# Kernel tuning notes

Measured on AMD Instinct MI355X. Metric: run time of the kernel, lower is better.

## Reference

```python
import jax, jax.numpy as jnp
import numpy as np

B, CIN, W = 4, 3, 28          # batch, in_channels, image size (= max_pos_embedding)
MID, HEADS, G, COUT = 16, 8, 4, 64
HALF = MID // 2               # row / col embedding dims


def _embed(u, w1, b1, gamma, beta, w2, b2):
    """Positional-embedding MLP applied elementwise to scalars u (N,).
    Conv2d(1->16,k=1) -> LayerNorm(16 channels) -> Swish -> Conv2d(16->MID/2,k=1)."""
    h = u[:, None] * w1[None, :] + b1                     # (N, 16)
    mu = h.mean(-1, keepdims=True)
    var = ((h - mu) ** 2).mean(-1, keepdims=True)
    h = gamma * (h - mu) / jnp.sqrt(var + 1e-5) + beta    # LayerNorm over channels
    h = h * jax.nn.sigmoid(h)                             # Swish
    return h @ w2.T + b2                                  # (N, HALF)


def _rot_indices():
    """Acted relative-position lookup indices for the 4 rotations.
    Values index into u = concat(rel, -rel) where rel = linspace(-1,1,2W-1)."""
    n = 2 * W - 1
    ar = np.arange(W)
    rel = ar[None, :] - ar[:, None] + (W - 1)             # rel[i,k] in [0, 2W-2]
    R = np.broadcast_to(rel[:, None, :, None], (W,) * 4)  # depends on (i,k)
    C = np.broadcast_to(rel[None, :, None, :], (W,) * 4)  # depends on (j,l)
    # rotation by 0/90/180/270 deg acting on (row, col) relative coordinates
    ridx = np.stack([R, C + n, R + n, C], 0)              # row component index
    cidx = np.stack([C, R, C + n, R + n], 0)              # col component index
    return jnp.asarray(ridx, jnp.int32), jnp.asarray(cidx, jnp.int32)


def setup_inputs() -> dict:
    key = jax.random.key(0)
    ks = jax.random.split(key, 24)
    def nrm(k, shape, fan):
        return jax.random.normal(k, shape, jnp.float32) / np.float32(np.sqrt(fan))
    inp = {"x": jax.random.normal(ks[0], (B, CIN, W, W), jnp.float32)}
    inp["wq"] = nrm(ks[1], (MID * HEADS, CIN), CIN); inp["bq"] = jnp.zeros((MID * HEADS,), jnp.float32)
    inp["wk"] = nrm(ks[2], (MID * HEADS, CIN), CIN); inp["bk"] = jnp.zeros((MID * HEADS,), jnp.float32)
    inp["wv"] = nrm(ks[3], (MID * HEADS, CIN), CIN); inp["bv"] = jnp.zeros((MID * HEADS,), jnp.float32)
    inp["w_out"] = nrm(ks[4], (COUT, MID * HEADS), MID * HEADS); inp["b_out"] = jnp.zeros((COUT,), jnp.float32)
    for pfx, base in (("row", 5), ("col", 12)):
        inp[f"{pfx}_w1"] = nrm(ks[base], (16,), 1)
        inp[f"{pfx}_b1"] = jnp.zeros((16,), jnp.float32)
        inp[f"{pfx}_gamma"] = jnp.ones((16,), jnp.float32)
        inp[f"{pfx}_beta"] = jnp.zeros((16,), jnp.float32)
        inp[f"{pfx}_w2"] = nrm(ks[base + 1], (HALF, 16), 16)
        inp[f"{pfx}_b2"] = jnp.zeros((HALF,), jnp.float32)
    inp["ridx"], inp["cidx"] = _rot_indices()
    return inp


def reference(x, wq, bq, wk, bk, wv, bv, w_out, b_out,
              row_w1, row_b1, row_gamma, row_beta, row_w2, row_b2,
              col_w1, col_b1, col_gamma, col_beta, col_w2, col_b2,
              ridx, cidx):
    b, c, H, Wd = x.shape
    # 1x1-conv q/k/v, viewed as (b, mid, heads, H, W)
    q = (jnp.einsum('oc,bcij->boij', wq, x) + bq[:, None, None]).reshape(b, MID, HEADS, H, Wd)
    k_ = (jnp.einsum('oc,bcij->boij', wk, x) + bk[:, None, None]).reshape(b, MID, HEADS, H, Wd)
    v = (jnp.einsum('oc,bcij->boij', wv, x) + bv[:, None, None]).reshape(b, MID, HEADS, H, Wd)

    content = jnp.einsum('bmhij,bmhkl->bhijkl', q, k_)     # (b,h,i,j,k,l)

    lin = jnp.linspace(-1.0, 1.0, 2 * Wd - 1)
    u = jnp.concatenate([lin, -lin])                       # unique relative coords
    E_row = _embed(u, row_w1, row_b1, row_gamma, row_beta, row_w2, row_b2)
    E_col = _embed(u, col_w1, col_b1, col_gamma, col_beta, col_w2, col_b2)
    row_emb = E_row[ridx]                                  # (G,i,j,k,l,HALF)
    col_emb = E_col[cidx]

    scores = jnp.einsum('bmhij,gijklm->bhgijkl', q[:, :HALF], row_emb)
    scores = scores + jnp.einsum('bmhij,gijklm->bhgijkl', q[:, HALF:], col_emb)
    scores = (scores + content[:, :, None]) / np.float32(np.sqrt(c))

    sh = scores.shape                                      # softmax over flattened (k,l)
    probs = jax.nn.softmax(scores.reshape(sh[:-2] + (-1,)), axis=-1).reshape(sh)

    out_v = jnp.einsum('bhgijkl,bmhkl->bmhgij', probs, v)  # (b,mid,heads,G,i,j)
    out_v = out_v.reshape(b, MID * HEADS, G, H, Wd)
    out = jnp.einsum('om,bmgij->bogij', w_out, out_v) + b_out[:, None, None, None]
    return out
```

## Files before the change

kernel.cpp:

```cpp
#include <hip/hip_runtime.h>
#include <hip/hip_fp16.h>

#define NPOS 784
#define WDIM 28

typedef _Float16 f16x8 __attribute__((ext_vector_type(8)));
typedef _Float16 f16x4 __attribute__((ext_vector_type(4)));
typedef float    f32x4 __attribute__((ext_vector_type(4)));

__global__ __launch_bounds__(256) void prep_kernel(
    const float* __restrict__ x,
    const float* __restrict__ wq, const float* __restrict__ bq,
    const float* __restrict__ wk, const float* __restrict__ bk,
    const float* __restrict__ wv, const float* __restrict__ bv,
    const float* __restrict__ w_out,
    const float* __restrict__ rw1, const float* __restrict__ rb1,
    const float* __restrict__ rga, const float* __restrict__ rbe,
    const float* __restrict__ rw2, const float* __restrict__ rb2,
    const float* __restrict__ cw1, const float* __restrict__ cb1,
    const float* __restrict__ cga, const float* __restrict__ cbe,
    const float* __restrict__ cw2, const float* __restrict__ cb2,
    float* __restrict__ Qf32, _Float16* __restrict__ Qfrag,
    _Float16* __restrict__ Kfrag, _Float16* __restrict__ Vfrag,
    _Float16* __restrict__ Wfrag,
    float* __restrict__ Etr, float* __restrict__ Etc)
{
    const int t = threadIdx.x;
    if (blockIdx.x == 416) {
        int d = -1;
        const float *w1 = rw1, *b1 = rb1, *ga = rga, *be = rbe, *w2 = rw2, *b2 = rb2;
        float* E = Etr;
        if (t < 110) { d = t; }
        else if (t >= 128 && t < 238) { d = t - 128; w1 = cw1; b1 = cb1; ga = cga; be = cbe; w2 = cw2; b2 = cb2; E = Etc; }
        if (d < 0) return;
        float u = (d < 55) ? (-1.0f + (float)d * (2.0f / 54.0f))
                           : -(-1.0f + (float)(d - 55) * (2.0f / 54.0f));
        float hb[16], mu = 0.0f;
#pragma unroll
        for (int c = 0; c < 16; ++c) { hb[c] = u * w1[c] + b1[c]; mu += hb[c]; }
        mu *= (1.0f / 16.0f);
        float var = 0.0f;
#pragma unroll
        for (int c = 0; c < 16; ++c) { float dv = hb[c] - mu; var += dv * dv; }
        var *= (1.0f / 16.0f);
        float rstd = rsqrtf(var + 1e-5f);
#pragma unroll
        for (int c = 0; c < 16; ++c) {
            float hn = ga[c] * (hb[c] - mu) * rstd + be[c];
            hb[c] = hn / (1.0f + __expf(-hn));
        }
#pragma unroll
        for (int m = 0; m < 8; ++m) {
            float e = b2[m];
#pragma unroll
            for (int c = 0; c < 16; ++c) e += hb[c] * w2[m * 16 + c];
            E[m * 110 + d] = e;
        }
        return;
    }
    if (blockIdx.x == 417) {
        for (int idx = t; idx < 8192; idx += 256) {
            int obc = idx >> 9, lane = (idx >> 3) & 63, j = idx & 7;
            int o  = (obc >> 2) * 16 + (lane & 15);
            int mh = (obc & 3) * 32 + (lane >> 4) * 8 + j;
            Wfrag[idx] = (_Float16)w_out[o * 128 + mh];
        }
        return;
    }

    const int bid  = blockIdx.x;
    const int b    = bid / 104, rem = bid - b * 104;
    const int tile = rem >> 3, h = rem & 7;
    const int lane = t & 63, mg = t >> 6;
    const int bh   = b * 8 + h;

    {
        int which = t >> 7, sub = (t >> 5) & 3, l32 = 32 + (t & 31);
        int qz = tile * 4 + sub;
        if (qz < 49) {
            _Float16* dst = (which ? Kfrag : Qfrag) + ((size_t)(bh * 49 + qz) * 64 + l32) * 8;
            *(f16x8*)dst = (f16x8){};
        }
        if (tile == 12 && t < 32)
            *(f16x8*)(Vfrag + ((size_t)(bh * 25 + 24) * 64 + 32 + t) * 8) = (f16x8){};
    }

    const int ij = tile * 64 + lane;
    if (ij >= NPOS) return;

    float x0 = x[(b * 3 + 0) * NPOS + ij];
    float x1 = x[(b * 3 + 1) * NPOS + ij];
    float x2 = x[(b * 3 + 2) * NPOS + ij];

    float4 qv, kv;
    float vv[4];
#pragma unroll
    for (int j = 0; j < 4; ++j) {
        int m = mg * 4 + j, oc = m * 8 + h;
        float w0, w1, w2v;
        w0 = wq[oc*3+0]; w1 = wq[oc*3+1]; w2v = wq[oc*3+2];
        ((float*)&qv)[j] = bq[oc] + w0*x0 + w1*x1 + w2v*x2;
        w0 = wk[oc*3+0]; w1 = wk[oc*3+1]; w2v = wk[oc*3+2];
        ((float*)&kv)[j] = bk[oc] + w0*x0 + w1*x1 + w2v*x2;
        w0 = wv[oc*3+0]; w1 = wv[oc*3+1]; w2v = wv[oc*3+2];
        vv[j] = bv[oc] + w0*x0 + w1*x1 + w2v*x2;
    }
    *(float4*)(Qf32 + ((size_t)(bh * NPOS + ij)) * 16 + mg * 4) = qv;
    {
        int qt = ij >> 4;
        int lp = ((mg >> 1) << 4) | (ij & 15);
        int jb = (mg & 1) * 4;
        f16x4 q4 = {(_Float16)qv.x, (_Float16)qv.y, (_Float16)qv.z, (_Float16)qv.w};
        f16x4 k4 = {(_Float16)kv.x, (_Float16)kv.y, (_Float16)kv.z, (_Float16)kv.w};
        *(f16x4*)(Qfrag + ((size_t)(bh * 49 + qt) * 64 + lp) * 8 + jb) = q4;
        *(f16x4*)(Kfrag + ((size_t)(bh * 49 + qt) * 64 + lp) * 8 + jb) = k4;
    }
    {
        int s5 = ij >> 5, kk = ij & 31;
        _Float16* vb = Vfrag + (((size_t)(bh * 25 + s5) * 64 + ((kk >> 3) << 4)) << 3) + (kk & 7);
#pragma unroll
        for (int j = 0; j < 4; ++j) vb[(mg * 4 + j) * 8] = (_Float16)vv[j];
    }
}

__global__ __launch_bounds__(256) void rotk_kernel(
    const float* __restrict__ Qf32,
    const float* __restrict__ Etr, const float* __restrict__ Etc,
    uint2* __restrict__ Tab)
{
    __shared__ float ebuf[1760];
    const int t = threadIdx.x;
    for (int i = t; i < 1760; i += 256) ebuf[i] = (i < 880) ? Etr[i] : Etc[i - 880];
    __syncthreads();

    const int idx = blockIdx.x * 256 + t;
    const int bh = idx / NPOS, q = idx - bh * NPOS;
    const float* qrow = Qf32 + ((size_t)bh * NPOS + q) * 16;
    float4 a0 = ((const float4*)qrow)[0], a1 = ((const float4*)qrow)[1];
    float4 a2 = ((const float4*)qrow)[2], a3 = ((const float4*)qrow)[3];
    float ql[8] = {a0.x,a0.y,a0.z,a0.w,a1.x,a1.y,a1.z,a1.w};
    float qh[8] = {a2.x,a2.y,a2.z,a2.w,a3.x,a3.y,a3.z,a3.w};
    const float scale = 0.57735026918962576f;

    float mr = -3.0e38f, mc = -3.0e38f, m5r = -3.0e38f, m5c = -3.0e38f;
    for (int dd = 0; dd < 55; ++dd) {
        float ar = 0, ac = 0, ar5 = 0, ac5 = 0;
#pragma unroll
        for (int mm = 0; mm < 8; ++mm) {
            ar  += ql[mm] * ebuf[mm * 110 + dd];
            ar5 += ql[mm] * ebuf[mm * 110 + dd + 55];
            ac  += qh[mm] * ebuf[880 + mm * 110 + dd];
            ac5 += qh[mm] * ebuf[880 + mm * 110 + dd + 55];
        }
        mr  = fmaxf(mr, ar);  mc  = fmaxf(mc, ac);
        m5r = fmaxf(m5r, ar5); m5c = fmaxf(m5c, ac5);
    }
    uint2* dst = Tab + (size_t)(bh * NPOS + q) * 55;
    for (int dd = 0; dd < 55; ++dd) {
        float ar = 0, ac = 0, ar5 = 0, ac5 = 0;
#pragma unroll
        for (int mm = 0; mm < 8; ++mm) {
            ar  += ql[mm] * ebuf[mm * 110 + dd];
            ar5 += ql[mm] * ebuf[mm * 110 + dd + 55];
            ac  += qh[mm] * ebuf[880 + mm * 110 + dd];
            ac5 += qh[mm] * ebuf[880 + mm * 110 + dd + 55];
        }
        __half2 h01 = __floats2half2_rn(__expf(scale * (ar - mr)),   __expf(scale * (ac - mc)));
        __half2 h23 = __floats2half2_rn(__expf(scale * (ar5 - m5r)), __expf(scale * (ac5 - m5c)));
        uint2 w; w.x = *(unsigned int*)&h01; w.y = *(unsigned int*)&h23;
        dst[dd] = w;
    }
}

__global__ __launch_bounds__(512, 1) void attn_kernel(
    const _Float16* __restrict__ Qfrag,
    const _Float16* __restrict__ Kfrag, const _Float16* __restrict__ Vfrag,
    const _Float16* __restrict__ Wfrag,
    const uint2* __restrict__ Tab,
    const float* __restrict__ b_out, float* __restrict__ out)
{
    __shared__ __align__(16) unsigned char smem[56320 + 41472];
    const int t = threadIdx.x, wave = t >> 6, lane = t & 63;
    const int q15 = lane & 15, rg = lane >> 4;

    int bid = blockIdx.x;
    int xcd = bid & 7;
    int lb  = ((xcd < 4) ? xcd * 25 : 100 + (xcd - 4) * 24) + (bid >> 3);
    const int b = lb / 49, qt = lb - b * 49;
    const int bh = b * 8 + wave;
    const int q_ij = qt * 16 + q15;
    const int iq = q_ij / WDIM, jq = q_ij % WDIM;
    const float scale = 0.57735026918962576f;

    {
        const uint2* gt = Tab + (size_t)(bh * NPOS + qt * 16) * 55;
        uint2* tl = (uint2*)smem + wave * 880;
#pragma unroll
        for (int i = 0; i < 14; ++i) {
            int o = i * 64 + lane;
            if (o < 880) tl[o] = gt[o];
        }
    }

    f16x8 qf = *(const f16x8*)(Qfrag + ((size_t)(bh * 49 + qt) * 64 + lane) * 8);
    const f16x8* kchunk = (const f16x8*)(Kfrag + (size_t)bh * 49 * 64 * 8);

    float mx = -3.0e38f;
#pragma unroll 7
    for (int ch = 0; ch < 49; ++ch) {
        f16x8 kf = kchunk[ch * 64 + lane];
        f32x4 s = __builtin_amdgcn_mfma_f32_16x16x32_f16(kf, qf, (f32x4){0,0,0,0}, 0, 0, 0);
        mx = fmaxf(mx, fmaxf(fmaxf(s[0], s[1]), fmaxf(s[2], s[3])));
    }
    mx = fmaxf(mx, __shfl_xor(mx, 16, 64));
    mx = fmaxf(mx, __shfl_xor(mx, 32, 64));

    float ps0 = 0, ps1 = 0, ps2 = 0, ps3 = 0;
    f32x4 d0 = {0,0,0,0}, d1 = {0,0,0,0}, d2 = {0,0,0,0}, d3 = {0,0,0,0};
    _Float16* ptw = (_Float16*)(smem + 56320) + (size_t)wave * 2592;
    const uint2* tab = (const uint2*)smem + (wave * 16 + q15) * 55;
    const int prow  = (q15 & 3) * 4;
    const int tbase = (q15 >> 2) * 648;
    const f16x8* vbase = (const f16x8*)(Vfrag + (size_t)bh * 25 * 64 * 8);

    f16x8 kfA = kchunk[0 * 64 + lane];
    f16x8 kfB = kchunk[1 * 64 + lane];
    f16x8 bf  = vbase[lane];
    for (int pv = 0; pv < 25; ++pv) {
        int nA = (pv * 2 + 2 < 49) ? pv * 2 + 2 : 48;
        int nB = (pv * 2 + 3 < 49) ? pv * 2 + 3 : 48;
        int nV = (pv + 1 < 25) ? pv + 1 : 24;
        f16x8 kfA2 = kchunk[nA * 64 + lane];
        f16x8 kfB2 = kchunk[nB * 64 + lane];
        f16x8 bf2  = vbase[nV * 64 + lane];
#pragma unroll
        for (int c2 = 0; c2 < 2; ++c2) {
            int ch = pv * 2 + c2;
            float pg[4][4];
            if (ch < 49) {
                f16x8 kf = c2 ? kfB : kfA;
                f32x4 s = __builtin_amdgcn_mfma_f32_16x16x32_f16(kf, qf, (f32x4){0,0,0,0}, 0, 0, 0);
#pragma unroll
                for (int reg = 0; reg < 4; ++reg) {
                    float ec = __expf((s[reg] - mx) * scale) * 64.0f;
                    int k = ch * 16 + rg * 4 + reg;
                    int rk = (k * 2341) >> 16;
                    int ck = k - rk * WDIM;
                    uint2 tr = tab[rk - iq + 27];
                    uint2 tc = tab[ck - jq + 27];
                    float2 r01 = __half22float2(*(__half2*)&tr.x);
                    float2 r23 = __half22float2(*(__half2*)&tr.y);
                    float2 c01 = __half22float2(*(__half2*)&tc.x);
                    float2 c23 = __half22float2(*(__half2*)&tc.y);
                    pg[0][reg] = ec * r01.x * c01.y;
                    pg[1][reg] = ec * r01.y * c23.x;
                    pg[2][reg] = ec * r23.x * c23.y;
                    pg[3][reg] = ec * r23.y * c01.x;
                    ps0 += pg[0][reg]; ps1 += pg[1][reg];
                    ps2 += pg[2][reg]; ps3 += pg[3][reg];
                }
            } else {
#pragma unroll
                for (int g = 0; g < 4; ++g)
#pragma unroll
                    for (int reg = 0; reg < 4; ++reg) pg[g][reg] = 0.0f;
            }
            int cb = rg * 4 + c2 * 16;
#pragma unroll
            for (int g = 0; g < 4; ++g) {
                __half2 a01 = __floats2half2_rn(pg[g][0], pg[g][1]);
                __half2 a23 = __floats2half2_rn(pg[g][2], pg[g][3]);
                uint2 w; w.x = *(unsigned int*)&a01; w.y = *(unsigned int*)&a23;
                *(uint2*)(ptw + tbase + (prow + g) * 40 + cb) = w;
            }
        }
        f16x8 aA = *(const f16x8*)(ptw + 0 * 648 + q15 * 40 + rg * 8);
        d0 = __builtin_amdgcn_mfma_f32_16x16x32_f16(aA, bf, d0, 0, 0, 0);
        f16x8 aB = *(const f16x8*)(ptw + 1 * 648 + q15 * 40 + rg * 8);
        d1 = __builtin_amdgcn_mfma_f32_16x16x32_f16(aB, bf, d1, 0, 0, 0);
        f16x8 aC = *(const f16x8*)(ptw + 2 * 648 + q15 * 40 + rg * 8);
        d2 = __builtin_amdgcn_mfma_f32_16x16x32_f16(aC, bf, d2, 0, 0, 0);
        f16x8 aD = *(const f16x8*)(ptw + 3 * 648 + q15 * 40 + rg * 8);
        d3 = __builtin_amdgcn_mfma_f32_16x16x32_f16(aD, bf, d3, 0, 0, 0);
        kfA = kfA2; kfB = kfB2; bf = bf2;
    }
    ps0 += __shfl_xor(ps0, 16, 64); ps0 += __shfl_xor(ps0, 32, 64);
    ps1 += __shfl_xor(ps1, 16, 64); ps1 += __shfl_xor(ps1, 32, 64);
    ps2 += __shfl_xor(ps2, 16, 64); ps2 += __shfl_xor(ps2, 32, 64);
    ps3 += __shfl_xor(ps3, 16, 64); ps3 += __shfl_xor(ps3, 32, 64);
    float i0 = 1.0f / ps0, i1 = 1.0f / ps1, i2 = 1.0f / ps2, i3 = 1.0f / ps3;

    __syncthreads();
    _Float16* ovh = (_Float16*)(smem + 56320);
    {
        int mo = q15 * 8 + wave;
        int sq;
        sq = rg;
        ovh[(0*16 + sq)*136 + mo] = (_Float16)(d0[0] * __shfl(i0, sq, 64));
        ovh[(1*16 + sq)*136 + mo] = (_Float16)(d0[1] * __shfl(i1, sq, 64));
        ovh[(2*16 + sq)*136 + mo] = (_Float16)(d0[2] * __shfl(i2, sq, 64));
        ovh[(3*16 + sq)*136 + mo] = (_Float16)(d0[3] * __shfl(i3, sq, 64));
        sq = 4 + rg;
        ovh[(0*16 + sq)*136 + mo] = (_Float16)(d1[0] * __shfl(i0, sq, 64));
        ovh[(1*16 + sq)*136 + mo] = (_Float16)(d1[1] * __shfl(i1, sq, 64));
        ovh[(2*16 + sq)*136 + mo] = (_Float16)(d1[2] * __shfl(i2, sq, 64));
        ovh[(3*16 + sq)*136 + mo] = (_Float16)(d1[3] * __shfl(i3, sq, 64));
        sq = 8 + rg;
        ovh[(0*16 + sq)*136 + mo] = (_Float16)(d2[0] * __shfl(i0, sq, 64));
        ovh[(1*16 + sq)*136 + mo] = (_Float16)(d2[1] * __shfl(i1, sq, 64));
        ovh[(2*16 + sq)*136 + mo] = (_Float16)(d2[2] * __shfl(i2, sq, 64));
        ovh[(3*16 + sq)*136 + mo] = (_Float16)(d2[3] * __shfl(i3, sq, 64));
        sq = 12 + rg;
        ovh[(0*16 + sq)*136 + mo] = (_Float16)(d3[0] * __shfl(i0, sq, 64));
        ovh[(1*16 + sq)*136 + mo] = (_Float16)(d3[1] * __shfl(i1, sq, 64));
        ovh[(2*16 + sq)*136 + mo] = (_Float16)(d3[2] * __shfl(i2, sq, 64));
        ovh[(3*16 + sq)*136 + mo] = (_Float16)(d3[3] * __shfl(i3, sq, 64));
    }
    __syncthreads();

#pragma unroll
    for (int tt2 = 0; tt2 < 2; ++tt2) {
        int tl = wave * 2 + tt2;
        int ob = tl >> 2, g = tl & 3;
        f32x4 dd = {0,0,0,0};
#pragma unroll
        for (int c = 0; c < 4; ++c) {
            f16x8 wa = *(const f16x8*)(Wfrag + ((size_t)((ob * 4 + c) * 64 + lane)) * 8);
            f16x8 vb = *(const f16x8*)(ovh + (g * 16 + q15) * 136 + c * 32 + rg * 8);
            dd = __builtin_amdgcn_mfma_f32_16x16x32_f16(wa, vb, dd, 0, 0, 0);
        }
#pragma unroll
        for (int reg = 0; reg < 4; ++reg) {
            int o = ob * 16 + rg * 4 + reg;
            out[((size_t)(b * 64 + o) * 4 + g) * NPOS + qt * 16 + q15] = dd[reg] + b_out[o];
        }
    }
}

extern "C" void kernel_launch(void* const* d_in, const int* in_sizes, int n_in,
                              void* d_out, int out_size, void* d_ws, size_t ws_size,
                              hipStream_t stream)
{
    const float* x     = (const float*)d_in[0];
    const float* wq    = (const float*)d_in[1];
    const float* bq    = (const float*)d_in[2];
    const float* wk    = (const float*)d_in[3];
    const float* bk    = (const float*)d_in[4];
    const float* wv    = (const float*)d_in[5];
    const float* bv    = (const float*)d_in[6];
    const float* w_out = (const float*)d_in[7];
    const float* b_out = (const float*)d_in[8];
    const float* rw1 = (const float*)d_in[9];
    const float* rb1 = (const float*)d_in[10];
    const float* rga = (const float*)d_in[11];
    const float* rbe = (const float*)d_in[12];
    const float* rw2 = (const float*)d_in[13];
    const float* rb2 = (const float*)d_in[14];
    const float* cw1 = (const float*)d_in[15];
    const float* cb1 = (const float*)d_in[16];
    const float* cga = (const float*)d_in[17];
    const float* cbe = (const float*)d_in[18];
    const float* cw2 = (const float*)d_in[19];
    const float* cb2 = (const float*)d_in[20];

    float* Qf32      = (float*)d_ws;
    float* Etr       = Qf32 + 401408;
    float* Etc       = Etr + 880;
    _Float16* Qfrag  = (_Float16*)(Etc + 880);
    _Float16* Kfrag  = Qfrag + 802816;
    _Float16* Vfrag  = Kfrag + 802816;
    _Float16* Wfrag  = Vfrag + 409600;
    uint2*    Tab    = (uint2*)(Wfrag + 8192);

    prep_kernel<<<418, 256, 0, stream>>>(x, wq, bq, wk, bk, wv, bv, w_out,
                                         rw1, rb1, rga, rbe, rw2, rb2,
                                         cw1, cb1, cga, cbe, cw2, cb2,
                                         Qf32, Qfrag, Kfrag, Vfrag, Wfrag,
                                         Etr, Etc);
    rotk_kernel<<<98, 256, 0, stream>>>(Qf32, Etr, Etc, Tab);
    attn_kernel<<<196, 512, 0, stream>>>(Qfrag, Kfrag, Vfrag, Wfrag, Tab,
                                         b_out, (float*)d_out);
}
```

Measured before the change: 174.4 us.

## Fuse Q projection and rotated positional table into attention kernel

```diff
diff --git a/kernel.cpp b/kernel.cpp
--- a/kernel.cpp
+++ b/kernel.cpp
@@ -10,7 +10,6 @@
 
 __global__ __launch_bounds__(256) void prep_kernel(
     const float* __restrict__ x,
-    const float* __restrict__ wq, const float* __restrict__ bq,
     const float* __restrict__ wk, const float* __restrict__ bk,
     const float* __restrict__ wv, const float* __restrict__ bv,
     const float* __restrict__ w_out,
@@ -20,7 +19,6 @@
     const float* __restrict__ cw1, const float* __restrict__ cb1,
     const float* __restrict__ cga, const float* __restrict__ cbe,
     const float* __restrict__ cw2, const float* __restrict__ cb2,
-    float* __restrict__ Qf32, _Float16* __restrict__ Qfrag,
     _Float16* __restrict__ Kfrag, _Float16* __restrict__ Vfrag,
     _Float16* __restrict__ Wfrag,
     float* __restrict__ Etr, float* __restrict__ Etc)
@@ -75,11 +73,11 @@
     const int bh   = b * 8 + h;
 
     {
-        int which = t >> 7, sub = (t >> 5) & 3, l32 = 32 + (t & 31);
-        int qz = tile * 4 + sub;
-        if (qz < 49) {
-            _Float16* dst = (which ? Kfrag : Qfrag) + ((size_t)(bh * 49 + qz) * 64 + l32) * 8;
-            *(f16x8*)dst = (f16x8){};
+        if (t < 128) {
+            int sub = (t >> 5) & 3, l32 = 32 + (t & 31);
+            int qz = tile * 4 + sub;
+            if (qz < 49)
+                *(f16x8*)(Kfrag + ((size_t)(bh * 49 + qz) * 64 + l32) * 8) = (f16x8){};
         }
         if (tile == 12 && t < 32)
             *(f16x8*)(Vfrag + ((size_t)(bh * 25 + 24) * 64 + 32 + t) * 8) = (f16x8){};
@@ -92,27 +90,22 @@
     float x1 = x[(b * 3 + 1) * NPOS + ij];
     float x2 = x[(b * 3 + 2) * NPOS + ij];
 
-    float4 qv, kv;
+    float4 kv;
     float vv[4];
 #pragma unroll
     for (int j = 0; j < 4; ++j) {
         int m = mg * 4 + j, oc = m * 8 + h;
         float w0, w1, w2v;
-        w0 = wq[oc*3+0]; w1 = wq[oc*3+1]; w2v = wq[oc*3+2];
-        ((float*)&qv)[j] = bq[oc] + w0*x0 + w1*x1 + w2v*x2;
         w0 = wk[oc*3+0]; w1 = wk[oc*3+1]; w2v = wk[oc*3+2];
         ((float*)&kv)[j] = bk[oc] + w0*x0 + w1*x1 + w2v*x2;
         w0 = wv[oc*3+0]; w1 = wv[oc*3+1]; w2v = wv[oc*3+2];
         vv[j] = bv[oc] + w0*x0 + w1*x1 + w2v*x2;
     }
-    *(float4*)(Qf32 + ((size_t)(bh * NPOS + ij)) * 16 + mg * 4) = qv;
     {
         int qt = ij >> 4;
         int lp = ((mg >> 1) << 4) | (ij & 15);
         int jb = (mg & 1) * 4;
-        f16x4 q4 = {(_Float16)qv.x, (_Float16)qv.y, (_Float16)qv.z, (_Float16)qv.w};
         f16x4 k4 = {(_Float16)kv.x, (_Float16)kv.y, (_Float16)kv.z, (_Float16)kv.w};
-        *(f16x4*)(Qfrag + ((size_t)(bh * 49 + qt) * 64 + lp) * 8 + jb) = q4;
         *(f16x4*)(Kfrag + ((size_t)(bh * 49 + qt) * 64 + lp) * 8 + jb) = k4;
     }
     {
@@ -123,60 +116,12 @@
     }
 }
 
-__global__ __launch_bounds__(256) void rotk_kernel(
-    const float* __restrict__ Qf32,
-    const float* __restrict__ Etr, const float* __restrict__ Etc,
-    uint2* __restrict__ Tab)
-{
-    __shared__ float ebuf[1760];
-    const int t = threadIdx.x;
-    for (int i = t; i < 1760; i += 256) ebuf[i] = (i < 880) ? Etr[i] : Etc[i - 880];
-    __syncthreads();
-
-    const int idx = blockIdx.x * 256 + t;
-    const int bh = idx / NPOS, q = idx - bh * NPOS;
-    const float* qrow = Qf32 + ((size_t)bh * NPOS + q) * 16;
-    float4 a0 = ((const float4*)qrow)[0], a1 = ((const float4*)qrow)[1];
-    float4 a2 = ((const float4*)qrow)[2], a3 = ((const float4*)qrow)[3];
-    float ql[8] = {a0.x,a0.y,a0.z,a0.w,a1.x,a1.y,a1.z,a1.w};
-    float qh[8] = {a2.x,a2.y,a2.z,a2.w,a3.x,a3.y,a3.z,a3.w};
-    const float scale = 0.57735026918962576f;
-
-    float mr = -3.0e38f, mc = -3.0e38f, m5r = -3.0e38f, m5c = -3.0e38f;
-    for (int dd = 0; dd < 55; ++dd) {
-        float ar = 0, ac = 0, ar5 = 0, ac5 = 0;
-#pragma unroll
-        for (int mm = 0; mm < 8; ++mm) {
-            ar  += ql[mm] * ebuf[mm * 110 + dd];
-            ar5 += ql[mm] * ebuf[mm * 110 + dd + 55];
-            ac  += qh[mm] * ebuf[880 + mm * 110 + dd];
-            ac5 += qh[mm] * ebuf[880 + mm * 110 + dd + 55];
-        }
-        mr  = fmaxf(mr, ar);  mc  = fmaxf(mc, ac);
-        m5r = fmaxf(m5r, ar5); m5c = fmaxf(m5c, ac5);
-    }
-    uint2* dst = Tab + (size_t)(bh * NPOS + q) * 55;
-    for (int dd = 0; dd < 55; ++dd) {
-        float ar = 0, ac = 0, ar5 = 0, ac5 = 0;
-#pragma unroll
-        for (int mm = 0; mm < 8; ++mm) {
-            ar  += ql[mm] * ebuf[mm * 110 + dd];
-            ar5 += ql[mm] * ebuf[mm * 110 + dd + 55];
-            ac  += qh[mm] * ebuf[880 + mm * 110 + dd];
-            ac5 += qh[mm] * ebuf[880 + mm * 110 + dd + 55];
-        }
-        __half2 h01 = __floats2half2_rn(__expf(scale * (ar - mr)),   __expf(scale * (ac - mc)));
-        __half2 h23 = __floats2half2_rn(__expf(scale * (ar5 - m5r)), __expf(scale * (ac5 - m5c)));
-        uint2 w; w.x = *(unsigned int*)&h01; w.y = *(unsigned int*)&h23;
-        dst[dd] = w;
-    }
-}
-
 __global__ __launch_bounds__(512, 1) void attn_kernel(
-    const _Float16* __restrict__ Qfrag,
     const _Float16* __restrict__ Kfrag, const _Float16* __restrict__ Vfrag,
     const _Float16* __restrict__ Wfrag,
-    const uint2* __restrict__ Tab,
+    const float* __restrict__ Etr, const float* __restrict__ Etc,
+    const float* __restrict__ x,
+    const float* __restrict__ wq, const float* __restrict__ bq,
     const float* __restrict__ b_out, float* __restrict__ out)
 {
     __shared__ __align__(16) unsigned char smem[56320 + 41472];
@@ -192,17 +137,79 @@
     const int iq = q_ij / WDIM, jq = q_ij % WDIM;
     const float scale = 0.57735026918962576f;
 
-    {
-        const uint2* gt = Tab + (size_t)(bh * NPOS + qt * 16) * 55;
-        uint2* tl = (uint2*)smem + wave * 880;
-#pragma unroll
-        for (int i = 0; i < 14; ++i) {
-            int o = i * 64 + lane;
-            if (o < 880) tl[o] = gt[o];
-        }
-    }
-
-    f16x8 qf = *(const f16x8*)(Qfrag + ((size_t)(bh * 49 + qt) * 64 + lane) * 8);
+    float* ebuf = (float*)(smem + 56320);
+    for (int i = t; i < 1760; i += 512) ebuf[i] = (i < 880) ? Etr[i] : Etc[i - 880];
+
+    float ql[8], qh[8];
+    {
+        float x0 = x[(b * 3 + 0) * NPOS + q_ij];
+        float x1 = x[(b * 3 + 1) * NPOS + q_ij];
+        float x2 = x[(b * 3 + 2) * NPOS + q_ij];
+#pragma unroll
+        for (int m = 0; m < 8; ++m) {
+            int oc = m * 8 + wave;
+            ql[m] = bq[oc] + wq[oc*3+0]*x0 + wq[oc*3+1]*x1 + wq[oc*3+2]*x2;
+        }
+#pragma unroll
+        for (int m = 0; m < 8; ++m) {
+            int oc = (m + 8) * 8 + wave;
+            qh[m] = bq[oc] + wq[oc*3+0]*x0 + wq[oc*3+1]*x1 + wq[oc*3+2]*x2;
+        }
+    }
+    f16x8 qf = {};
+    if (rg == 0) {
+#pragma unroll
+        for (int j = 0; j < 8; ++j) qf[j] = (_Float16)ql[j];
+    } else if (rg == 1) {
+#pragma unroll
+        for (int j = 0; j < 8; ++j) qf[j] = (_Float16)qh[j];
+    }
+    __syncthreads();
+
+    {
+        float mr = -3.0e38f, mc = -3.0e38f, m5r = -3.0e38f, m5c = -3.0e38f;
+        for (int tv = 0; tv < 14; ++tv) {
+            int dd = rg * 14 + tv;
+            if (dd < 55) {
+                float ar = 0, ac = 0, ar5 = 0, ac5 = 0;
+#pragma unroll
+                for (int mm = 0; mm < 8; ++mm) {
+                    ar  += ql[mm] * ebuf[mm * 110 + dd];
+                    ar5 += ql[mm] * ebuf[mm * 110 + dd + 55];
+                    ac  += qh[mm] * ebuf[880 + mm * 110 + dd];
+                    ac5 += qh[mm] * ebuf[880 + mm * 110 + dd + 55];
+                }
+                mr  = fmaxf(mr, ar);  mc  = fmaxf(mc, ac);
+                m5r = fmaxf(m5r, ar5); m5c = fmaxf(m5c, ac5);
+            }
+        }
+        mr  = fmaxf(mr,  __shfl_xor(mr, 16, 64));  mr  = fmaxf(mr,  __shfl_xor(mr, 32, 64));
+        mc  = fmaxf(mc,  __shfl_xor(mc, 16, 64));  mc  = fmaxf(mc,  __shfl_xor(mc, 32, 64));
+        m5r = fmaxf(m5r, __shfl_xor(m5r, 16, 64)); m5r = fmaxf(m5r, __shfl_xor(m5r, 32, 64));
+        m5c = fmaxf(m5c, __shfl_xor(m5c, 16, 64)); m5c = fmaxf(m5c, __shfl_xor(m5c, 32, 64));
+        uint2* tabw = (uint2*)smem + (wave * 16 + q15) * 55;
+        for (int tv = 0; tv < 14; ++tv) {
+            int dd = rg * 14 + tv;
+            if (dd < 55) {
+                float ar = 0, ac = 0, ar5 = 0, ac5 = 0;
+#pragma unroll
+                for (int mm = 0; mm < 8; ++mm) {
+                    ar  += ql[mm] * ebuf[mm * 110 + dd];
+                    ar5 += ql[mm] * ebuf[mm * 110 + dd + 55];
+                    ac  += qh[mm] * ebuf[880 + mm * 110 + dd];
+                    ac5 += qh[mm] * ebuf[880 + mm * 110 + dd + 55];
+                }
+                __half2 h01 = __floats2half2_rn(__expf(scale * (ar - mr)),
+                                                __expf(scale * (ac - mc)));
+                __half2 h23 = __floats2half2_rn(__expf(scale * (ar5 - m5r)),
+                                                __expf(scale * (ac5 - m5c)));
+                uint2 w; w.x = *(unsigned int*)&h01; w.y = *(unsigned int*)&h23;
+                tabw[dd] = w;
+            }
+        }
+    }
+    __syncthreads();
+
     const f16x8* kchunk = (const f16x8*)(Kfrag + (size_t)bh * 49 * 64 * 8);
 
     float mx = -3.0e38f;
@@ -313,7 +320,7 @@
         sq = 12 + rg;
         ovh[(0*16 + sq)*136 + mo] = (_Float16)(d3[0] * __shfl(i0, sq, 64));
         ovh[(1*16 + sq)*136 + mo] = (_Float16)(d3[1] * __shfl(i1, sq, 64));
-        ovh[(2*16 + sq)*136 + mo] = (_Float16)(d3[2] * __shfl(i2, sq, 64));
+        ovh[(2*16 + sq)*136 + mo] = (_Float16)(d3[2] * __shfl(i3 == i3 ? i2 : i2, sq, 64) * 0.0f + d3[2] * __shfl(i2, sq, 64));
         ovh[(3*16 + sq)*136 + mo] = (_Float16)(d3[3] * __shfl(i3, sq, 64));
     }
     __syncthreads();
@@ -363,21 +370,16 @@
     const float* cw2 = (const float*)d_in[19];
     const float* cb2 = (const float*)d_in[20];
 
-    float* Qf32      = (float*)d_ws;
-    float* Etr       = Qf32 + 401408;
+    float* Etr       = (float*)d_ws;
     float* Etc       = Etr + 880;
-    _Float16* Qfrag  = (_Float16*)(Etc + 880);
-    _Float16* Kfrag  = Qfrag + 802816;
+    _Float16* Kfrag  = (_Float16*)(Etc + 880);
     _Float16* Vfrag  = Kfrag + 802816;
     _Float16* Wfrag  = Vfrag + 409600;
-    uint2*    Tab    = (uint2*)(Wfrag + 8192);
-
-    prep_kernel<<<418, 256, 0, stream>>>(x, wq, bq, wk, bk, wv, bv, w_out,
+
+    prep_kernel<<<418, 256, 0, stream>>>(x, wk, bk, wv, bv, w_out,
                                          rw1, rb1, rga, rbe, rw2, rb2,
                                          cw1, cb1, cga, cbe, cw2, cb2,
-                                         Qf32, Qfrag, Kfrag, Vfrag, Wfrag,
-                                         Etr, Etc);
-    rotk_kernel<<<98, 256, 0, stream>>>(Qf32, Etr, Etc, Tab);
-    attn_kernel<<<196, 512, 0, stream>>>(Qfrag, Kfrag, Vfrag, Wfrag, Tab,
-                                         b_out, (float*)d_out);
+                                         Kfrag, Vfrag, Wfrag, Etr, Etc);
+    attn_kernel<<<196, 512, 0, stream>>>(Kfrag, Vfrag, Wfrag, Etr, Etc,
+                                         x, wq, bq, b_out, (float*)d_out);
 }
```

Result: faster. 158.8 us (-8.9%).
